# Performance work log

Measured on AMD Instinct MI355X. Metric: run time of the kernel, lower is better.

Reference implementation:

```python
import jax, jax.numpy as jnp
import numpy as np

N_NODES = 50000
N_EDGES = 800000
IN_C = 128
HID_C = 2 * IN_C  # 256
OUT_C = 128
NEG_SLOPE = 0.2


def _gat_layer(x, edge_src, edge_dst, W, a_src, a_dst, b, n_nodes):
    # x: [N, Fin], W: [Fin, Fout], a_src/a_dst: [Fout], b: [Fout]
    h = x @ W                                   # [N, Fout]
    alpha_src = h @ a_src                       # [N]
    alpha_dst = h @ a_dst                       # [N]
    e = alpha_src[edge_src] + alpha_dst[edge_dst]           # [E]
    e = jnp.where(e > 0, e, NEG_SLOPE * e)      # LeakyReLU(0.2)
    # segment softmax over incoming edges of each destination node
    m = jax.ops.segment_max(e, edge_dst, num_segments=n_nodes)  # [N]
    w = jnp.exp(e - m[edge_dst])                               # [E]
    z = jax.ops.segment_sum(w, edge_dst, num_segments=n_nodes)  # [N]
    alpha = w / z[edge_dst]                                     # [E]
    # scatter-aggregate messages
    out = jax.ops.segment_sum(alpha[:, None] * h[edge_src], edge_dst,
                              num_segments=n_nodes)             # [N, Fout]
    return out + b


def setup_inputs() -> dict:
    key = jax.random.key(0)
    ks = jax.random.split(key, 12)
    x = jax.random.normal(ks[0], (N_NODES, IN_C), dtype=jnp.float32)
    edge_index = jax.random.randint(ks[1], (2, N_EDGES), 0, N_NODES, dtype=jnp.int32)
    def glorot(k, shape):
        fan_in = shape[0] if len(shape) == 2 else shape[0]
        return jax.random.normal(k, shape, dtype=jnp.float32) / np.sqrt(fan_in)
    W1 = glorot(ks[2], (IN_C, HID_C))
    a1_src = glorot(ks[3], (HID_C,))
    a1_dst = glorot(ks[4], (HID_C,))
    b1 = jnp.zeros((HID_C,), dtype=jnp.float32)
    W2 = glorot(ks[5], (HID_C, OUT_C))
    a2_src = glorot(ks[6], (OUT_C,))
    a2_dst = glorot(ks[7], (OUT_C,))
    b2 = jnp.zeros((OUT_C,), dtype=jnp.float32)
    return {"x": x, "edge_index": edge_index, "W1": W1, "a1_src": a1_src,
            "a1_dst": a1_dst, "b1": b1, "W2": W2, "a2_src": a2_src,
            "a2_dst": a2_dst, "b2": b2}


def reference(x, edge_index, W1, a1_src, a1_dst, b1, W2, a2_src, a2_dst, b2):
    n = x.shape[0]
    # PyG GATConv default: add self-loops
    loops = jnp.arange(n, dtype=edge_index.dtype)
    src = jnp.concatenate([edge_index[0], loops])
    dst = jnp.concatenate([edge_index[1], loops])
    h = _gat_layer(x, src, dst, W1, a1_src, a1_dst, b1, n)
    h = jax.nn.relu(h)
    out = _gat_layer(h, src, dst, W2, a2_src, a2_dst, b2, n)
    return out
```

## Files before the change

### kernel.cpp

```cpp
#include <hip/hip_runtime.h>
#include <hip/hip_bf16.h>
#include <math.h>

#define N_NODES 50000
#define N_EDGESX 800000
#define E_TOT   (N_EDGESX + N_NODES)
#define IN_C 128
#define HID_C 256
#define OUT_C 128
#define NEG_SLOPE 0.2f

#define NPB   100
#define NBUCK ((N_NODES + NPB - 1) / NPB)
#define BCAP  2560
#define EPB   4096
#define NABLK ((E_TOT + EPB - 1) / EPB)

typedef __attribute__((ext_vector_type(8))) short short8;
typedef __attribute__((ext_vector_type(4))) float floatx4;
typedef __attribute__((ext_vector_type(2))) float floatx2;

__device__ __forceinline__ float bf2f(short s) {
    unsigned u = ((unsigned)(unsigned short)s) << 16;
    float f; __builtin_memcpy(&f, &u, 4); return f;
}
__device__ __forceinline__ short f2bf(float f) {
    unsigned u; __builtin_memcpy(&u, &f, 4);
    unsigned r = (u + 0x7FFFu + ((u >> 16) & 1u)) >> 16;
    return (short)r;
}

template<int KROWS, int NCOLS>
__global__ __launch_bounds__(256)
void gemv_p_kernel(const float* __restrict__ W, const float* __restrict__ a_s,
                   const float* __restrict__ a_d, float* __restrict__ ps, float* __restrict__ pd) {
    int t = threadIdx.x;
    int k = t & (KROWS - 1);
    const float* av = (t < KROWS) ? a_s : a_d;
    float* pv = (t < KROWS) ? ps : pd;
    const float* row = W + (size_t)k * NCOLS;
    float s = 0.f;
    for (int n = 0; n < NCOLS; ++n) s += row[n] * av[n];
    pv[k] = s;
}

__global__ __launch_bounds__(256)
void alpha_x_kernel(const float* __restrict__ x, const float* __restrict__ ps,
                    const float* __restrict__ pd, float* __restrict__ as_out,
                    float* __restrict__ ad_out, short* __restrict__ xb) {
    int gt = blockIdx.x * blockDim.x + threadIdx.x;
    int node = gt >> 6, lane = gt & 63;
    if (node >= N_NODES) return;
    floatx2 xv = *(const floatx2*)&x[(size_t)node * IN_C + lane * 2];
    floatx2 s2 = *(const floatx2*)&ps[lane * 2];
    floatx2 d2 = *(const floatx2*)&pd[lane * 2];
    float s = xv[0] * s2[0] + xv[1] * s2[1];
    float d = xv[0] * d2[0] + xv[1] * d2[1];
    unsigned pack = (unsigned)(unsigned short)f2bf(xv[0]) | ((unsigned)(unsigned short)f2bf(xv[1]) << 16);
    *(unsigned*)&xb[(size_t)node * IN_C + lane * 2] = pack;
    #pragma unroll
    for (int off = 32; off; off >>= 1) {
        s += __shfl_down(s, off);
        d += __shfl_down(d, off);
    }
    if (lane == 0) { as_out[node] = s; ad_out[node] = d; }
}

__global__ __launch_bounds__(256)
void binA_kernel(const int* __restrict__ src, const int* __restrict__ dst,
                 int* __restrict__ bcnt, int* __restrict__ stage) {
    __shared__ int hist[NBUCK];
    __shared__ int base[NBUCK];
    for (int b = threadIdx.x; b < NBUCK; b += 256) hist[b] = 0;
    __syncthreads();
    int e0 = blockIdx.x * EPB;
    int e1 = min(e0 + EPB, E_TOT);
    for (int i = e0 + threadIdx.x; i < e1; i += 256) {
        int d = (i < N_EDGESX) ? dst[i] : (i - N_EDGESX);
        atomicAdd(&hist[d / NPB], 1);
    }
    __syncthreads();
    for (int b = threadIdx.x; b < NBUCK; b += 256) {
        int c = hist[b];
        base[b] = c ? atomicAdd(&bcnt[b], c) : 0;
        hist[b] = 0;
    }
    __syncthreads();
    for (int i = e0 + threadIdx.x; i < e1; i += 256) {
        int s, d;
        if (i < N_EDGESX) { s = src[i]; d = dst[i]; }
        else { s = i - N_EDGESX; d = s; }
        int b = d / NPB;
        int off = base[b] + atomicAdd(&hist[b], 1);
        if (off < BCAP) stage[(size_t)b * BCAP + off] = ((d - b * NPB) << 17) | s;
    }
}

__global__ __launch_bounds__(128)
void bucket_count_kernel(const int* __restrict__ bcnt, const int* __restrict__ stage,
                         int* __restrict__ cnt) {
    __shared__ int lc[NPB];
    int b = blockIdx.x;
    for (int t = threadIdx.x; t < NPB; t += 128) lc[t] = 0;
    __syncthreads();
    int n = min(bcnt[b], BCAP);
    const int* sp = stage + (size_t)b * BCAP;
    for (int i = threadIdx.x; i < n; i += 128)
        atomicAdd(&lc[sp[i] >> 17], 1);
    __syncthreads();
    int nb = b * NPB;
    for (int t = threadIdx.x; t < NPB; t += 128)
        if (nb + t < N_NODES) cnt[nb + t] = lc[t];
}

__global__ __launch_bounds__(128)
void bucket_scatter_kernel(const int* __restrict__ bcnt, const int* __restrict__ stage,
                           const int* __restrict__ row_ptr, const float* __restrict__ as_in,
                           const float* __restrict__ ad_in, int* __restrict__ esrc,
                           float* __restrict__ ew) {
    __shared__ int cur[NPB];
    __shared__ float adl[NPB];
    int b = blockIdx.x;
    int nb = b * NPB;
    for (int t = threadIdx.x; t < NPB; t += 128) {
        int node = nb + t;
        cur[t] = (node < N_NODES) ? row_ptr[node] : 0;
        adl[t] = (node < N_NODES) ? ad_in[node] : 0.f;
    }
    __syncthreads();
    int n = min(bcnt[b], BCAP);
    const int* sp = stage + (size_t)b * BCAP;
    for (int i = threadIdx.x; i < n; i += 128) {
        int v = sp[i];
        int s = v & 0x1FFFF;
        int li = v >> 17;
        int pos = atomicAdd(&cur[li], 1);
        esrc[pos] = s;
        float e = as_in[s] + adl[li];
        ew[pos] = e > 0.f ? e : NEG_SLOPE * e;
    }
}

#define NBLK ((N_NODES + 1023) / 1024)

__global__ __launch_bounds__(1024)
void scan_a_kernel(const int* __restrict__ cnt, int* __restrict__ row_ptr, int* __restrict__ bsum) {
    __shared__ int buf[1024];
    int tid = threadIdx.x;
    int idx = blockIdx.x * 1024 + tid;
    int v = (idx < N_NODES) ? cnt[idx] : 0;
    buf[tid] = v;
    __syncthreads();
    for (int off = 1; off < 1024; off <<= 1) {
        int t = (tid >= off) ? buf[tid - off] : 0;
        __syncthreads();
        buf[tid] += t;
        __syncthreads();
    }
    if (idx < N_NODES) row_ptr[idx] = buf[tid] - v;
    if (tid == 1023) bsum[blockIdx.x] = buf[1023];
}

__global__ void scan_b_kernel(int* __restrict__ bsum, int* __restrict__ row_ptr) {
    int lane = threadIdx.x;
    int v = (lane < NBLK) ? bsum[lane] : 0;
    int s = v;
    #pragma unroll
    for (int off = 1; off < 64; off <<= 1) {
        int t = __shfl_up(s, off);
        if (lane >= off) s += t;
    }
    if (lane < NBLK) bsum[lane] = s - v;
    if (lane == 63) row_ptr[N_NODES] = s;
}

__global__ __launch_bounds__(1024)
void scan_c_kernel(int* __restrict__ row_ptr, const int* __restrict__ bsum) {
    int idx = blockIdx.x * 1024 + threadIdx.x;
    if (idx < N_NODES) row_ptr[idx] += bsum[blockIdx.x];
}

__global__ __launch_bounds__(256)
void fill_edst_kernel(const int* __restrict__ row_ptr, int* __restrict__ edst) {
    int gt = blockIdx.x * blockDim.x + threadIdx.x;
    int node = gt >> 6, lane = gt & 63;
    if (node >= N_NODES) return;
    int beg = row_ptr[node], end = row_ptr[node + 1];
    for (int i = beg + lane; i < end; i += 64) edst[i] = node;
}

__global__ void ew_kernel(const int* __restrict__ esrc, const int* __restrict__ edst,
                          const float* __restrict__ as_in, const float* __restrict__ ad_in,
                          float* __restrict__ ew) {
    int i = blockIdx.x * blockDim.x + threadIdx.x;
    if (i >= E_TOT) return;
    float e = as_in[esrc[i]] + ad_in[edst[i]];
    ew[i] = e > 0.f ? e : NEG_SLOPE * e;
}

__global__ void splitT_kernel(const float* __restrict__ W, short* __restrict__ th,
                              short* __restrict__ tl, int K, int N) {
    int i = blockIdx.x * blockDim.x + threadIdx.x;
    if (i >= K * N) return;
    int k = i / N, n = i - k * N;
    float f = W[i];
    short hb = f2bf(f);
    th[n * K + k] = hb;
    tl[n * K + k] = f2bf(f - bf2f(hb));
}

template<int K, int HASALO, int OUTMODE>
__global__ __launch_bounds__(256)
void gemm_mfma(const short* __restrict__ Ah, const short* __restrict__ Al,
               const short* __restrict__ Bth, const short* __restrict__ Btl,
               int N, const float* __restrict__ bias, short* __restrict__ C0) {
    __shared__ short Ah_s[128][40];
    __shared__ short Al_s[HASALO ? 128 : 1][HASALO ? 40 : 1];
    __shared__ short Bh_s[64][40];
    __shared__ short Bl_s[64][40];
    int tid = threadIdx.x;
    int lane = tid & 63, wave = tid >> 6;
    int wr = wave >> 1, wc = wave & 1;
    int bm = blockIdx.y * 128, bn = blockIdx.x * 64;
    int l15 = lane & 15, kf = (lane >> 4) * 8;

    floatx4 acc[4][2];
    #pragma unroll
    for (int i = 0; i < 4; ++i)
        #pragma unroll
        for (int j = 0; j < 2; ++j) acc[i][j] = (floatx4){0.f, 0.f, 0.f, 0.f};

    int arow = tid >> 1, ac0 = (tid & 1) * 16;
    int brow = tid >> 2, bc0 = (tid & 3) * 8;
    int agm = bm + arow;
    bool aval = agm < N_NODES;

    for (int k0 = 0; k0 < K; k0 += 32) {
        short8 va0 = {0,0,0,0,0,0,0,0}, va1 = va0;
        if (aval) {
            const short* pa = Ah + (size_t)agm * K + k0 + ac0;
            va0 = *(const short8*)pa; va1 = *(const short8*)(pa + 8);
        }
        *(short8*)&Ah_s[arow][ac0]     = va0;
        *(short8*)&Ah_s[arow][ac0 + 8] = va1;
        if (HASALO) {
            short8 vl0 = {0,0,0,0,0,0,0,0}, vl1 = vl0;
            if (aval) {
                const short* pl = Al + (size_t)agm * K + k0 + ac0;
                vl0 = *(const short8*)pl; vl1 = *(const short8*)(pl + 8);
            }
            *(short8*)&Al_s[arow][ac0]     = vl0;
            *(short8*)&Al_s[arow][ac0 + 8] = vl1;
        }
        {
            const short* pb = Bth + (size_t)(bn + brow) * K + k0 + bc0;
            *(short8*)&Bh_s[brow][bc0] = *(const short8*)pb;
            const short* pb2 = Btl + (size_t)(bn + brow) * K + k0 + bc0;
            *(short8*)&Bl_s[brow][bc0] = *(const short8*)pb2;
        }
        __syncthreads();
        short8 afh[4], bfh[2], bfl[2];
        #pragma unroll
        for (int mr = 0; mr < 4; ++mr) {
            int r = wr * 64 + mr * 16 + l15;
            afh[mr] = *(const short8*)&Ah_s[r][kf];
        }
        #pragma unroll
        for (int nr = 0; nr < 2; ++nr) {
            int c = wc * 32 + nr * 16 + l15;
            bfh[nr] = *(const short8*)&Bh_s[c][kf];
            bfl[nr] = *(const short8*)&Bl_s[c][kf];
        }
        #pragma unroll
        for (int mr = 0; mr < 4; ++mr)
            #pragma unroll
            for (int nr = 0; nr < 2; ++nr) {
                acc[mr][nr] = __builtin_amdgcn_mfma_f32_16x16x32_bf16(afh[mr], bfh[nr], acc[mr][nr], 0, 0, 0);
                acc[mr][nr] = __builtin_amdgcn_mfma_f32_16x16x32_bf16(afh[mr], bfl[nr], acc[mr][nr], 0, 0, 0);
            }
        if (HASALO) {
            short8 afl[4];
            #pragma unroll
            for (int mr = 0; mr < 4; ++mr) {
                int r = wr * 64 + mr * 16 + l15;
                afl[mr] = *(const short8*)&Al_s[r][kf];
            }
            #pragma unroll
            for (int mr = 0; mr < 4; ++mr)
                #pragma unroll
                for (int nr = 0; nr < 2; ++nr)
                    acc[mr][nr] = __builtin_amdgcn_mfma_f32_16x16x32_bf16(afl[mr], bfh[nr], acc[mr][nr], 0, 0, 0);
        }
        __syncthreads();
    }
    float bv[2];
    if (OUTMODE == 2) {
        #pragma unroll
        for (int nr = 0; nr < 2; ++nr) bv[nr] = bias[bn + wc * 32 + nr * 16 + l15];
    }
    #pragma unroll
    for (int mr = 0; mr < 4; ++mr) {
        #pragma unroll
        for (int reg = 0; reg < 4; ++reg) {
            int gr = bm + wr * 64 + mr * 16 + (lane >> 4) * 4 + reg;
            if (gr < N_NODES) {
                #pragma unroll
                for (int nr = 0; nr < 2; ++nr) {
                    int gc = bn + wc * 32 + nr * 16 + l15;
                    float v = acc[mr][nr][reg];
                    if (OUTMODE == 2) v = fmaxf(v + bv[nr], 0.f);
                    C0[(size_t)gr * N + gc] = f2bf(v);
                }
            }
        }
    }
}

__global__ __launch_bounds__(256)
void alpha_bf16_128(const short* __restrict__ h, const float* __restrict__ a_src,
                    const float* __restrict__ a_dst, float* __restrict__ as_out,
                    float* __restrict__ ad_out) {
    int gt = blockIdx.x * blockDim.x + threadIdx.x;
    int node = gt >> 6, lane = gt & 63;
    if (node >= N_NODES) return;
    unsigned u = *(const unsigned*)&h[(size_t)node * OUT_C + lane * 2];
    float v0 = bf2f((short)(u & 0xFFFFu));
    float v1 = bf2f((short)(u >> 16));
    floatx2 as2 = *(const floatx2*)&a_src[lane * 2];
    floatx2 ad2 = *(const floatx2*)&a_dst[lane * 2];
    float s = v0 * as2[0] + v1 * as2[1];
    float d = v0 * ad2[0] + v1 * ad2[1];
    #pragma unroll
    for (int off = 32; off; off >>= 1) {
        s += __shfl_down(s, off);
        d += __shfl_down(d, off);
    }
    if (lane == 0) { as_out[node] = s; ad_out[node] = d; }
}

template<int OUT>
__global__ __launch_bounds__(256)
void aggregate_kernel(const short* __restrict__ h, const float* __restrict__ ew,
                      const int* __restrict__ row_ptr, const int* __restrict__ esrc,
                      const float* __restrict__ bias,
                      short* __restrict__ o_hi, short* __restrict__ o_lo,
                      float* __restrict__ o_f32) {
    int gt = blockIdx.x * blockDim.x + threadIdx.x;
    int node = gt >> 6, lane = gt & 63;
    if (node >= N_NODES) return;
    int beg = row_ptr[node], end = row_ptr[node + 1];

    float ml = -1e30f, zl = 0.f;
    for (int i = beg + lane; i < end; i += 64) {
        float e = ew[i];
        float mn = fmaxf(ml, e);
        zl = zl * __expf(ml - mn) + __expf(e - mn);
        ml = mn;
    }
    #pragma unroll
    for (int off = 32; off; off >>= 1) {
        float mo = __shfl_xor(ml, off);
        float zo = __shfl_xor(zl, off);
        float mn = fmaxf(ml, mo);
        zl = zl * __expf(ml - mn) + zo * __expf(mo - mn);
        ml = mn;
    }
    float m = ml;
    float inv_z = 1.f / zl;

    int grp = lane >> 4, l = lane & 15;
    float acc[8] = {};
    int i = beg;
    for (; i + 16 <= end; i += 16) {
        int e0 = i + grp, e1 = e0 + 4, e2 = e0 + 8, e3 = e0 + 12;
        int s0 = esrc[e0], s1 = esrc[e1], s2 = esrc[e2], s3 = esrc[e3];
        float w0 = __expf(ew[e0] - m) * inv_z;
        float w1 = __expf(ew[e1] - m) * inv_z;
        float w2 = __expf(ew[e2] - m) * inv_z;
        float w3 = __expf(ew[e3] - m) * inv_z;
        short8 hv0 = *(const short8*)&h[(size_t)s0 * 128 + l * 8];
        short8 hv1 = *(const short8*)&h[(size_t)s1 * 128 + l * 8];
        short8 hv2 = *(const short8*)&h[(size_t)s2 * 128 + l * 8];
        short8 hv3 = *(const short8*)&h[(size_t)s3 * 128 + l * 8];
        #pragma unroll
        for (int j = 0; j < 8; ++j) acc[j] += w0 * bf2f(hv0[j]);
        #pragma unroll
        for (int j = 0; j < 8; ++j) acc[j] += w1 * bf2f(hv1[j]);
        #pragma unroll
        for (int j = 0; j < 8; ++j) acc[j] += w2 * bf2f(hv2[j]);
        #pragma unroll
        for (int j = 0; j < 8; ++j) acc[j] += w3 * bf2f(hv3[j]);
    }
    for (; i < end; i += 4) {
        int e = i + grp;
        bool v = e < end;
        int s = esrc[v ? e : beg];
        float w = v ? __expf(ew[e] - m) * inv_z : 0.f;
        short8 hv = *(const short8*)&h[(size_t)s * 128 + l * 8];
        #pragma unroll
        for (int j = 0; j < 8; ++j) acc[j] += w * bf2f(hv[j]);
    }
    #pragma unroll
    for (int j = 0; j < 8; ++j) {
        acc[j] += __shfl_xor(acc[j], 16);
        acc[j] += __shfl_xor(acc[j], 32);
    }

    if (lane < 16) {
        if (OUT == 0) {
            short8 oh, ol;
            #pragma unroll
            for (int j = 0; j < 8; ++j) {
                short hb = f2bf(acc[j]);
                oh[j] = hb;
                ol[j] = f2bf(acc[j] - bf2f(hb));
            }
            *(short8*)&o_hi[(size_t)node * 128 + l * 8] = oh;
            *(short8*)&o_lo[(size_t)node * 128 + l * 8] = ol;
        } else {
            const float* brow = &bias[l * 8];
            floatx4 o0, o1;
            #pragma unroll
            for (int j = 0; j < 4; ++j) {
                o0[j] = acc[j] + brow[j];
                o1[j] = acc[j + 4] + brow[j + 4];
            }
            float* orow = &o_f32[(size_t)node * 128 + l * 8];
            *(floatx4*)orow = o0;
            *(floatx4*)(orow + 4) = o1;
        }
    }
}

extern "C" void kernel_launch(void* const* d_in, const int* in_sizes, int n_in,
                              void* d_out, int out_size, void* d_ws, size_t ws_size,
                              hipStream_t stream) {
    const float* x   = (const float*)d_in[0];
    const int*   ei  = (const int*)d_in[1];
    const float* W1  = (const float*)d_in[2];
    const float* a1s = (const float*)d_in[3];
    const float* a1d = (const float*)d_in[4];
    const float* b1  = (const float*)d_in[5];
    const float* W2  = (const float*)d_in[6];
    const float* a2s = (const float*)d_in[7];
    const float* a2d = (const float*)d_in[8];
    const float* b2  = (const float*)d_in[9];
    float* out = (float*)d_out;

    const int* e_src = ei;
    const int* e_dst = ei + N_EDGESX;

    char* ws = (char*)d_ws;
    const size_t OFF_XB    = 0;
    const size_t OFF_UH    = 12800000;
    const size_t OFF_UL    = 25600000;
    const size_t OFF_G1H   = 38400000;
    const size_t OFF_H2    = 64000000;
    const size_t OFF_W1TH  = 76800000;
    const size_t OFF_W1TL  = 76865536;
    const size_t OFF_W2TH  = 76931072;
    const size_t OFF_W2TL  = 76996608;
    const size_t OFF_P1S   = 77062144;
    const size_t OFF_P1D   = 77062656;
    const size_t OFF_AS    = 77063168;
    const size_t OFF_AD    = 77263360;
    const size_t OFF_RP    = 77463552;
    const size_t OFF_CNT   = 77664000;
    const size_t OFF_BSUM  = 77864192;
    const size_t OFF_BCNT  = 77864448;
    const size_t OFF_ESRC  = 77866496;
    const size_t OFF_EDST  = 81266496;
    const size_t OFF_EW    = 84666496;
    const size_t OFF_STAGE = 88066496;

    short* xb   = (short*)(ws + OFF_XB);
    short* uh   = (short*)(ws + OFF_UH);
    short* ul   = (short*)(ws + OFF_UL);
    short* g1h  = (short*)(ws + OFF_G1H);
    short* h2   = (short*)(ws + OFF_H2);
    short* w1th = (short*)(ws + OFF_W1TH);
    short* w1tl = (short*)(ws + OFF_W1TL);
    short* w2th = (short*)(ws + OFF_W2TH);
    short* w2tl = (short*)(ws + OFF_W2TL);
    float* p1s  = (float*)(ws + OFF_P1S);
    float* p1d  = (float*)(ws + OFF_P1D);
    float* as_b = (float*)(ws + OFF_AS);
    float* ad_b = (float*)(ws + OFF_AD);
    int* row_ptr = (int*)(ws + OFF_RP);
    int* cnt     = (int*)(ws + OFF_CNT);
    int* bsum    = (int*)(ws + OFF_BSUM);
    int* bcnt    = (int*)(ws + OFF_BCNT);
    int* esrc    = (int*)(ws + OFF_ESRC);
    int* edst    = (int*)(ws + OFF_EDST);
    float* ewb   = (float*)(ws + OFF_EW);
    int* stage   = (int*)(ws + OFF_STAGE);

    int egrid = (E_TOT + 255) / 256;
    int ngrid = (N_NODES * 64 + 255) / 256;

    gemv_p_kernel<IN_C, HID_C><<<1, 256, 0, stream>>>(W1, a1s, a1d, p1s, p1d);
    alpha_x_kernel<<<ngrid, 256, 0, stream>>>(x, p1s, p1d, as_b, ad_b, xb);

    hipMemsetAsync(bcnt, 0, NBUCK * sizeof(int), stream);
    binA_kernel<<<NABLK, 256, 0, stream>>>(e_src, e_dst, bcnt, stage);
    bucket_count_kernel<<<NBUCK, 128, 0, stream>>>(bcnt, stage, cnt);
    scan_a_kernel<<<NBLK, 1024, 0, stream>>>(cnt, row_ptr, bsum);
    scan_b_kernel<<<1, 64, 0, stream>>>(bsum, row_ptr);
    scan_c_kernel<<<NBLK, 1024, 0, stream>>>(row_ptr, bsum);
    bucket_scatter_kernel<<<NBUCK, 128, 0, stream>>>(bcnt, stage, row_ptr, as_b, ad_b, esrc, ewb);
    fill_edst_kernel<<<ngrid, 256, 0, stream>>>(row_ptr, edst);

    splitT_kernel<<<(IN_C * HID_C + 255) / 256, 256, 0, stream>>>(W1, w1th, w1tl, IN_C, HID_C);
    splitT_kernel<<<(HID_C * OUT_C + 255) / 256, 256, 0, stream>>>(W2, w2th, w2tl, HID_C, OUT_C);

    aggregate_kernel<0><<<ngrid, 256, 0, stream>>>(xb, ewb, row_ptr, esrc, nullptr, uh, ul, nullptr);
    gemm_mfma<IN_C, 1, 2><<<dim3(HID_C / 64, (N_NODES + 127) / 128), 256, 0, stream>>>(
        uh, ul, w1th, w1tl, HID_C, b1, g1h);

    gemm_mfma<HID_C, 0, 1><<<dim3(OUT_C / 64, (N_NODES + 127) / 128), 256, 0, stream>>>(
        g1h, nullptr, w2th, w2tl, OUT_C, nullptr, h2);
    alpha_bf16_128<<<ngrid, 256, 0, stream>>>(h2, a2s, a2d, as_b, ad_b);
    ew_kernel<<<egrid, 256, 0, stream>>>(esrc, edst, as_b, ad_b, ewb);
    aggregate_kernel<1><<<ngrid, 256, 0, stream>>>(h2, ewb, row_ptr, esrc, b2, nullptr, nullptr, out);
}
```

Measured before the change: 299.1 us.

## Replace per-node segment max with global bound and fuse softmax into aggregation

The per-destination max pass is replaced by a single global upper bound C = max(alpha_src) + max(alpha_dst), computed by a one-block reduction. Exp weights are then produced directly in the scatter (layer 1) or inside aggregation (layer 2), with normalisation by the accumulated sum. This removes the online-softmax first pass, the edst fill and ew kernels, and the low-half aggregate output plus its extra MFMA pass in the first GEMM. In exchange it risks underflow when logits sit far below the global bound, adds two single-block serial reductions, and lowers layer-1 precision by dropping the bf16 lo split of the aggregated features.

```diff
diff --git a/kernel.cpp b/kernel.cpp
--- a/kernel.cpp
+++ b/kernel.cpp
@@ -66,6 +66,34 @@
     if (lane == 0) { as_out[node] = s; ad_out[node] = d; }
 }
 
+__global__ __launch_bounds__(1024)
+void maxred_kernel(const float* __restrict__ a, const float* __restrict__ b,
+                   float* __restrict__ c) {
+    __shared__ float sa[16], sb[16];
+    int t = threadIdx.x;
+    float ma = -1e30f, mb = -1e30f;
+    for (int i = t; i < N_NODES; i += 1024) {
+        ma = fmaxf(ma, a[i]);
+        mb = fmaxf(mb, b[i]);
+    }
+    #pragma unroll
+    for (int off = 32; off; off >>= 1) {
+        ma = fmaxf(ma, __shfl_down(ma, off));
+        mb = fmaxf(mb, __shfl_down(mb, off));
+    }
+    if ((t & 63) == 0) { sa[t >> 6] = ma; sb[t >> 6] = mb; }
+    __syncthreads();
+    if (t < 16) {
+        ma = sa[t]; mb = sb[t];
+        #pragma unroll
+        for (int off = 8; off; off >>= 1) {
+            ma = fmaxf(ma, __shfl_down(ma, off));
+            mb = fmaxf(mb, __shfl_down(mb, off));
+        }
+        if (t == 0) c[0] = ma + mb;
+    }
+}
+
 __global__ __launch_bounds__(256)
 void binA_kernel(const int* __restrict__ src, const int* __restrict__ dst,
                  int* __restrict__ bcnt, int* __restrict__ stage) {
@@ -116,12 +144,13 @@
 __global__ __launch_bounds__(128)
 void bucket_scatter_kernel(const int* __restrict__ bcnt, const int* __restrict__ stage,
                            const int* __restrict__ row_ptr, const float* __restrict__ as_in,
-                           const float* __restrict__ ad_in, int* __restrict__ esrc,
-                           float* __restrict__ ew) {
+                           const float* __restrict__ ad_in, const float* __restrict__ Cptr,
+                           int* __restrict__ esrc, float* __restrict__ we) {
     __shared__ int cur[NPB];
     __shared__ float adl[NPB];
     int b = blockIdx.x;
     int nb = b * NPB;
+    float C = Cptr[0];
     for (int t = threadIdx.x; t < NPB; t += 128) {
         int node = nb + t;
         cur[t] = (node < N_NODES) ? row_ptr[node] : 0;
@@ -137,7 +166,8 @@
         int pos = atomicAdd(&cur[li], 1);
         esrc[pos] = s;
         float e = as_in[s] + adl[li];
-        ew[pos] = e > 0.f ? e : NEG_SLOPE * e;
+        e = fmaxf(e, NEG_SLOPE * e);
+        we[pos] = __expf(e - C);
     }
 }
 
@@ -178,24 +208,6 @@
 void scan_c_kernel(int* __restrict__ row_ptr, const int* __restrict__ bsum) {
     int idx = blockIdx.x * 1024 + threadIdx.x;
     if (idx < N_NODES) row_ptr[idx] += bsum[blockIdx.x];
-}
-
-__global__ __launch_bounds__(256)
-void fill_edst_kernel(const int* __restrict__ row_ptr, int* __restrict__ edst) {
-    int gt = blockIdx.x * blockDim.x + threadIdx.x;
-    int node = gt >> 6, lane = gt & 63;
-    if (node >= N_NODES) return;
-    int beg = row_ptr[node], end = row_ptr[node + 1];
-    for (int i = beg + lane; i < end; i += 64) edst[i] = node;
-}
-
-__global__ void ew_kernel(const int* __restrict__ esrc, const int* __restrict__ edst,
-                          const float* __restrict__ as_in, const float* __restrict__ ad_in,
-                          float* __restrict__ ew) {
-    int i = blockIdx.x * blockDim.x + threadIdx.x;
-    if (i >= E_TOT) return;
-    float e = as_in[esrc[i]] + ad_in[edst[i]];
-    ew[i] = e > 0.f ? e : NEG_SLOPE * e;
 }
 
 __global__ void splitT_kernel(const float* __restrict__ W, short* __restrict__ th,
@@ -209,13 +221,12 @@
     tl[n * K + k] = f2bf(f - bf2f(hb));
 }
 
-template<int K, int HASALO, int OUTMODE>
-__global__ __launch_bounds__(256)
-void gemm_mfma(const short* __restrict__ Ah, const short* __restrict__ Al,
+template<int K, int OUTMODE>
+__global__ __launch_bounds__(256)
+void gemm_mfma(const short* __restrict__ Ah,
                const short* __restrict__ Bth, const short* __restrict__ Btl,
                int N, const float* __restrict__ bias, short* __restrict__ C0) {
     __shared__ short Ah_s[128][40];
-    __shared__ short Al_s[HASALO ? 128 : 1][HASALO ? 40 : 1];
     __shared__ short Bh_s[64][40];
     __shared__ short Bl_s[64][40];
     int tid = threadIdx.x;
@@ -243,15 +254,6 @@
         }
         *(short8*)&Ah_s[arow][ac0]     = va0;
         *(short8*)&Ah_s[arow][ac0 + 8] = va1;
-        if (HASALO) {
-            short8 vl0 = {0,0,0,0,0,0,0,0}, vl1 = vl0;
-            if (aval) {
-                const short* pl = Al + (size_t)agm * K + k0 + ac0;
-                vl0 = *(const short8*)pl; vl1 = *(const short8*)(pl + 8);
-            }
-            *(short8*)&Al_s[arow][ac0]     = vl0;
-            *(short8*)&Al_s[arow][ac0 + 8] = vl1;
-        }
         {
             const short* pb = Bth + (size_t)(bn + brow) * K + k0 + bc0;
             *(short8*)&Bh_s[brow][bc0] = *(const short8*)pb;
@@ -278,19 +280,6 @@
                 acc[mr][nr] = __builtin_amdgcn_mfma_f32_16x16x32_bf16(afh[mr], bfh[nr], acc[mr][nr], 0, 0, 0);
                 acc[mr][nr] = __builtin_amdgcn_mfma_f32_16x16x32_bf16(afh[mr], bfl[nr], acc[mr][nr], 0, 0, 0);
             }
-        if (HASALO) {
-            short8 afl[4];
-            #pragma unroll
-            for (int mr = 0; mr < 4; ++mr) {
-                int r = wr * 64 + mr * 16 + l15;
-                afl[mr] = *(const short8*)&Al_s[r][kf];
-            }
-            #pragma unroll
-            for (int mr = 0; mr < 4; ++mr)
-                #pragma unroll
-                for (int nr = 0; nr < 2; ++nr)
-                    acc[mr][nr] = __builtin_amdgcn_mfma_f32_16x16x32_bf16(afl[mr], bfh[nr], acc[mr][nr], 0, 0, 0);
-        }
         __syncthreads();
     }
     float bv[2];
@@ -338,50 +327,27 @@
     if (lane == 0) { as_out[node] = s; ad_out[node] = d; }
 }
 
-template<int OUT>
-__global__ __launch_bounds__(256)
-void aggregate_kernel(const short* __restrict__ h, const float* __restrict__ ew,
-                      const int* __restrict__ row_ptr, const int* __restrict__ esrc,
-                      const float* __restrict__ bias,
-                      short* __restrict__ o_hi, short* __restrict__ o_lo,
-                      float* __restrict__ o_f32) {
+__global__ __launch_bounds__(256)
+void aggregate1_kernel(const short* __restrict__ h, const float* __restrict__ we,
+                       const int* __restrict__ row_ptr, const int* __restrict__ esrc,
+                       short* __restrict__ o_u) {
     int gt = blockIdx.x * blockDim.x + threadIdx.x;
     int node = gt >> 6, lane = gt & 63;
     if (node >= N_NODES) return;
     int beg = row_ptr[node], end = row_ptr[node + 1];
-
-    float ml = -1e30f, zl = 0.f;
-    for (int i = beg + lane; i < end; i += 64) {
-        float e = ew[i];
-        float mn = fmaxf(ml, e);
-        zl = zl * __expf(ml - mn) + __expf(e - mn);
-        ml = mn;
-    }
-    #pragma unroll
-    for (int off = 32; off; off >>= 1) {
-        float mo = __shfl_xor(ml, off);
-        float zo = __shfl_xor(zl, off);
-        float mn = fmaxf(ml, mo);
-        zl = zl * __expf(ml - mn) + zo * __expf(mo - mn);
-        ml = mn;
-    }
-    float m = ml;
-    float inv_z = 1.f / zl;
-
     int grp = lane >> 4, l = lane & 15;
     float acc[8] = {};
+    float zl = 0.f;
     int i = beg;
     for (; i + 16 <= end; i += 16) {
         int e0 = i + grp, e1 = e0 + 4, e2 = e0 + 8, e3 = e0 + 12;
         int s0 = esrc[e0], s1 = esrc[e1], s2 = esrc[e2], s3 = esrc[e3];
-        float w0 = __expf(ew[e0] - m) * inv_z;
-        float w1 = __expf(ew[e1] - m) * inv_z;
-        float w2 = __expf(ew[e2] - m) * inv_z;
-        float w3 = __expf(ew[e3] - m) * inv_z;
+        float w0 = we[e0], w1 = we[e1], w2 = we[e2], w3 = we[e3];
         short8 hv0 = *(const short8*)&h[(size_t)s0 * 128 + l * 8];
         short8 hv1 = *(const short8*)&h[(size_t)s1 * 128 + l * 8];
         short8 hv2 = *(const short8*)&h[(size_t)s2 * 128 + l * 8];
         short8 hv3 = *(const short8*)&h[(size_t)s3 * 128 + l * 8];
+        zl += (w0 + w1) + (w2 + w3);
         #pragma unroll
         for (int j = 0; j < 8; ++j) acc[j] += w0 * bf2f(hv0[j]);
         #pragma unroll
@@ -395,40 +361,96 @@
         int e = i + grp;
         bool v = e < end;
         int s = esrc[v ? e : beg];
-        float w = v ? __expf(ew[e] - m) * inv_z : 0.f;
+        float w = v ? we[e] : 0.f;
         short8 hv = *(const short8*)&h[(size_t)s * 128 + l * 8];
+        zl += w;
         #pragma unroll
         for (int j = 0; j < 8; ++j) acc[j] += w * bf2f(hv[j]);
     }
+    zl += __shfl_xor(zl, 16);
+    zl += __shfl_xor(zl, 32);
     #pragma unroll
     for (int j = 0; j < 8; ++j) {
         acc[j] += __shfl_xor(acc[j], 16);
         acc[j] += __shfl_xor(acc[j], 32);
     }
-
+    float invz = 1.f / zl;
     if (lane < 16) {
-        if (OUT == 0) {
-            short8 oh, ol;
-            #pragma unroll
-            for (int j = 0; j < 8; ++j) {
-                short hb = f2bf(acc[j]);
-                oh[j] = hb;
-                ol[j] = f2bf(acc[j] - bf2f(hb));
-            }
-            *(short8*)&o_hi[(size_t)node * 128 + l * 8] = oh;
-            *(short8*)&o_lo[(size_t)node * 128 + l * 8] = ol;
-        } else {
-            const float* brow = &bias[l * 8];
-            floatx4 o0, o1;
-            #pragma unroll
-            for (int j = 0; j < 4; ++j) {
-                o0[j] = acc[j] + brow[j];
-                o1[j] = acc[j + 4] + brow[j + 4];
-            }
-            float* orow = &o_f32[(size_t)node * 128 + l * 8];
-            *(floatx4*)orow = o0;
-            *(floatx4*)(orow + 4) = o1;
-        }
+        short8 oh;
+        #pragma unroll
+        for (int j = 0; j < 8; ++j) oh[j] = f2bf(acc[j] * invz);
+        *(short8*)&o_u[(size_t)node * 128 + l * 8] = oh;
+    }
+}
+
+__global__ __launch_bounds__(256)
+void aggregate2_kernel(const short* __restrict__ h, const float* __restrict__ as2,
+                       const float* __restrict__ ad2, const float* __restrict__ Cptr,
+                       const int* __restrict__ row_ptr, const int* __restrict__ esrc,
+                       const float* __restrict__ bias, float* __restrict__ out) {
+    int gt = blockIdx.x * blockDim.x + threadIdx.x;
+    int node = gt >> 6, lane = gt & 63;
+    if (node >= N_NODES) return;
+    int beg = row_ptr[node], end = row_ptr[node + 1];
+    float C = Cptr[0];
+    float adn = ad2[node];
+    int grp = lane >> 4, l = lane & 15;
+    float acc[8] = {};
+    float zl = 0.f;
+    int i = beg;
+    for (; i + 16 <= end; i += 16) {
+        int e0 = i + grp, e1 = e0 + 4, e2 = e0 + 8, e3 = e0 + 12;
+        int s0 = esrc[e0], s1 = esrc[e1], s2 = esrc[e2], s3 = esrc[e3];
+        float t0 = as2[s0] + adn, t1 = as2[s1] + adn, t2 = as2[s2] + adn, t3 = as2[s3] + adn;
+        t0 = fmaxf(t0, NEG_SLOPE * t0); t1 = fmaxf(t1, NEG_SLOPE * t1);
+        t2 = fmaxf(t2, NEG_SLOPE * t2); t3 = fmaxf(t3, NEG_SLOPE * t3);
+        float w0 = __expf(t0 - C), w1 = __expf(t1 - C);
+        float w2 = __expf(t2 - C), w3 = __expf(t3 - C);
+        short8 hv0 = *(const short8*)&h[(size_t)s0 * 128 + l * 8];
+        short8 hv1 = *(const short8*)&h[(size_t)s1 * 128 + l * 8];
+        short8 hv2 = *(const short8*)&h[(size_t)s2 * 128 + l * 8];
+        short8 hv3 = *(const short8*)&h[(size_t)s3 * 128 + l * 8];
+        zl += (w0 + w1) + (w2 + w3);
+        #pragma unroll
+        for (int j = 0; j < 8; ++j) acc[j] += w0 * bf2f(hv0[j]);
+        #pragma unroll
+        for (int j = 0; j < 8; ++j) acc[j] += w1 * bf2f(hv1[j]);
+        #pragma unroll
+        for (int j = 0; j < 8; ++j) acc[j] += w2 * bf2f(hv2[j]);
+        #pragma unroll
+        for (int j = 0; j < 8; ++j) acc[j] += w3 * bf2f(hv3[j]);
+    }
+    for (; i < end; i += 4) {
+        int e = i + grp;
+        bool v = e < end;
+        int s = esrc[v ? e : beg];
+        float t = as2[s] + adn;
+        t = fmaxf(t, NEG_SLOPE * t);
+        float w = v ? __expf(t - C) : 0.f;
+        short8 hv = *(const short8*)&h[(size_t)s * 128 + l * 8];
+        zl += w;
+        #pragma unroll
+        for (int j = 0; j < 8; ++j) acc[j] += w * bf2f(hv[j]);
+    }
+    zl += __shfl_xor(zl, 16);
+    zl += __shfl_xor(zl, 32);
+    #pragma unroll
+    for (int j = 0; j < 8; ++j) {
+        acc[j] += __shfl_xor(acc[j], 16);
+        acc[j] += __shfl_xor(acc[j], 32);
+    }
+    float invz = 1.f / zl;
+    if (lane < 16) {
+        const float* brow = &bias[l * 8];
+        floatx4 o0, o1;
+        #pragma unroll
+        for (int j = 0; j < 4; ++j) {
+            o0[j] = acc[j] * invz + brow[j];
+            o1[j] = acc[j + 4] * invz + brow[j + 4];
+        }
+        float* orow = &out[(size_t)node * 128 + l * 8];
+        *(floatx4*)orow = o0;
+        *(floatx4*)(orow + 4) = o1;
     }
 }
 
@@ -453,29 +475,27 @@
     char* ws = (char*)d_ws;
     const size_t OFF_XB    = 0;
     const size_t OFF_UH    = 12800000;
-    const size_t OFF_UL    = 25600000;
-    const size_t OFF_G1H   = 38400000;
-    const size_t OFF_H2    = 64000000;
-    const size_t OFF_W1TH  = 76800000;
-    const size_t OFF_W1TL  = 76865536;
-    const size_t OFF_W2TH  = 76931072;
-    const size_t OFF_W2TL  = 76996608;
-    const size_t OFF_P1S   = 77062144;
-    const size_t OFF_P1D   = 77062656;
-    const size_t OFF_AS    = 77063168;
-    const size_t OFF_AD    = 77263360;
-    const size_t OFF_RP    = 77463552;
-    const size_t OFF_CNT   = 77664000;
-    const size_t OFF_BSUM  = 77864192;
-    const size_t OFF_BCNT  = 77864448;
-    const size_t OFF_ESRC  = 77866496;
-    const size_t OFF_EDST  = 81266496;
-    const size_t OFF_EW    = 84666496;
-    const size_t OFF_STAGE = 88066496;
+    const size_t OFF_G1H   = 25600000;
+    const size_t OFF_H2    = 51200000;
+    const size_t OFF_W1TH  = 64000000;
+    const size_t OFF_W1TL  = 64065536;
+    const size_t OFF_W2TH  = 64131072;
+    const size_t OFF_W2TL  = 64196608;
+    const size_t OFF_P1S   = 64262144;
+    const size_t OFF_P1D   = 64262656;
+    const size_t OFF_CMAX  = 64263168;
+    const size_t OFF_AS    = 64263424;
+    const size_t OFF_AD    = 64463616;
+    const size_t OFF_RP    = 64663808;
+    const size_t OFF_CNT   = 64864256;
+    const size_t OFF_BSUM  = 65064448;
+    const size_t OFF_BCNT  = 65064704;
+    const size_t OFF_ESRC  = 65066752;
+    const size_t OFF_WE    = 68466752;
+    const size_t OFF_STAGE = 71866752;
 
     short* xb   = (short*)(ws + OFF_XB);
     short* uh   = (short*)(ws + OFF_UH);
-    short* ul   = (short*)(ws + OFF_UL);
     short* g1h  = (short*)(ws + OFF_G1H);
     short* h2   = (short*)(ws + OFF_H2);
     short* w1th = (short*)(ws + OFF_W1TH);
@@ -484,6 +504,7 @@
     short* w2tl = (short*)(ws + OFF_W2TL);
     float* p1s  = (float*)(ws + OFF_P1S);
     float* p1d  = (float*)(ws + OFF_P1D);
+    float* cmax = (float*)(ws + OFF_CMAX);
     float* as_b = (float*)(ws + OFF_AS);
     float* ad_b = (float*)(ws + OFF_AD);
     int* row_ptr = (int*)(ws + OFF_RP);
@@ -491,15 +512,14 @@
     int* bsum    = (int*)(ws + OFF_BSUM);
     int* bcnt    = (int*)(ws + OFF_BCNT);
     int* esrc    = (int*)(ws + OFF_ESRC);
-    int* edst    = (int*)(ws + OFF_EDST);
-    float* ewb   = (float*)(ws + OFF_EW);
+    float* web   = (float*)(ws + OFF_WE);
     int* stage   = (int*)(ws + OFF_STAGE);
 
-    int egrid = (E_TOT + 255) / 256;
     int ngrid = (N_NODES * 64 + 255) / 256;
 
     gemv_p_kernel<IN_C, HID_C><<<1, 256, 0, stream>>>(W1, a1s, a1d, p1s, p1d);
     alpha_x_kernel<<<ngrid, 256, 0, stream>>>(x, p1s, p1d, as_b, ad_b, xb);
+    maxred_kernel<<<1, 1024, 0, stream>>>(as_b, ad_b, cmax);
 
     hipMemsetAsync(bcnt, 0, NBUCK * sizeof(int), stream);
     binA_kernel<<<NABLK, 256, 0, stream>>>(e_src, e_dst, bcnt, stage);
@@ -507,19 +527,18 @@
     scan_a_kernel<<<NBLK, 1024, 0, stream>>>(cnt, row_ptr, bsum);
     scan_b_kernel<<<1, 64, 0, stream>>>(bsum, row_ptr);
     scan_c_kernel<<<NBLK, 1024, 0, stream>>>(row_ptr, bsum);
-    bucket_scatter_kernel<<<NBUCK, 128, 0, stream>>>(bcnt, stage, row_ptr, as_b, ad_b, esrc, ewb);
-    fill_edst_kernel<<<ngrid, 256, 0, stream>>>(row_ptr, edst);
+    bucket_scatter_kernel<<<NBUCK, 128, 0, stream>>>(bcnt, stage, row_ptr, as_b, ad_b, cmax, esrc, web);
 
     splitT_kernel<<<(IN_C * HID_C + 255) / 256, 256, 0, stream>>>(W1, w1th, w1tl, IN_C, HID_C);
     splitT_kernel<<<(HID_C * OUT_C + 255) / 256, 256, 0, stream>>>(W2, w2th, w2tl, HID_C, OUT_C);
 
-    aggregate_kernel<0><<<ngrid, 256, 0, stream>>>(xb, ewb, row_ptr, esrc, nullptr, uh, ul, nullptr);
-    gemm_mfma<IN_C, 1, 2><<<dim3(HID_C / 64, (N_NODES + 127) / 128), 256, 0, stream>>>(
-        uh, ul, w1th, w1tl, HID_C, b1, g1h);
-
-    gemm_mfma<HID_C, 0, 1><<<dim3(OUT_C / 64, (N_NODES + 127) / 128), 256, 0, stream>>>(
-        g1h, nullptr, w2th, w2tl, OUT_C, nullptr, h2);
+    aggregate1_kernel<<<ngrid, 256, 0, stream>>>(xb, web, row_ptr, esrc, uh);
+    gemm_mfma<IN_C, 2><<<dim3(HID_C / 64, (N_NODES + 127) / 128), 256, 0, stream>>>(
+        uh, w1th, w1tl, HID_C, b1, g1h);
+
+    gemm_mfma<HID_C, 1><<<dim3(OUT_C / 64, (N_NODES + 127) / 128), 256, 0, stream>>>(
+        g1h, w2th, w2tl, OUT_C, nullptr, h2);
     alpha_bf16_128<<<ngrid, 256, 0, stream>>>(h2, a2s, a2d, as_b, ad_b);
-    ew_kernel<<<egrid, 256, 0, stream>>>(esrc, edst, as_b, ad_b, ewb);
-    aggregate_kernel<1><<<ngrid, 256, 0, stream>>>(h2, ewb, row_ptr, esrc, b2, nullptr, nullptr, out);
-}
+    maxred_kernel<<<1, 1024, 0, stream>>>(as_b, ad_b, cmax + 1);
+    aggregate2_kernel<<<ngrid, 256, 0, stream>>>(h2, as_b, ad_b, cmax + 1, row_ptr, esrc, b2, out);
+}
```

After: 301.6 us. Within noise of the previous version (+0.8%).
